# Optimization experiments

Hardware: AMD Instinct MI355X
Metric: run time of the kernel (lower is better)

## Reference

```python
import jax, jax.numpy as jnp
import numpy as np

VOCAB = 28996
B, W, D, H = 16, 64, 256, 512


def setup_inputs() -> dict:
    key = jax.random.key(0)
    ks = jax.random.split(key, 8)
    s_ih = 1.0 / np.sqrt(H)
    return {
        "x": jax.random.normal(ks[0], (B, W, D), dtype=jnp.float32),
        "last_encoder_hidden_state": jax.random.normal(ks[1], (1, H), dtype=jnp.float32),
        "w_ih": jax.random.uniform(ks[2], (3 * H, D), jnp.float32, -s_ih, s_ih),
        "w_hh": jax.random.uniform(ks[3], (3 * H, H), jnp.float32, -s_ih, s_ih),
        "b_ih": jax.random.uniform(ks[4], (3 * H,), jnp.float32, -s_ih, s_ih),
        "b_hh": jax.random.uniform(ks[5], (3 * H,), jnp.float32, -s_ih, s_ih),
        "w_pred": jax.random.uniform(ks[6], (VOCAB, H), jnp.float32, -s_ih, s_ih),
        "b_pred": jax.random.uniform(ks[7], (VOCAB,), jnp.float32, -s_ih, s_ih),
    }


def reference(x, last_encoder_hidden_state, w_ih, w_hh, b_ih, b_hh, w_pred, b_pred):
    b, w, d = x.shape
    # The torch code carries a single [1,H] hidden state sequentially over ALL
    # batch rows and words (state flows across batch boundaries). Flatten to T steps.
    xf = x.reshape(b * w, d)
    xg = xf @ w_ih.T + b_ih  # [T, 3H] input gate pre-activations, batched GEMM

    def step(h, xg_t):
        gh = h @ w_hh.T + b_hh            # [3H]
        xr, xz, xn = jnp.split(xg_t, 3)
        hr, hz, hn = jnp.split(gh, 3)
        r = jax.nn.sigmoid(xr + hr)
        z = jax.nn.sigmoid(xz + hz)
        n = jnp.tanh(xn + r * hn)
        h_new = (1.0 - z) * n + z * h
        return h_new, h_new

    h0 = last_encoder_hidden_state[0]     # [H]
    _, hs = jax.lax.scan(step, h0, xg)    # hs: [T, H]
    preds = hs @ w_pred.T + b_pred        # [T, VOCAB]
    return preds.reshape(b, w, VOCAB)
```

## Files before the change

### kernel.cpp

```cpp
#include <hip/hip_runtime.h>
#include <hip/hip_bf16.h>
#include <cstdint>

#define VOCAB 28996
#define T_STEPS 1024
#define D_IN 256
#define HDIM 512

using f32x4 = __attribute__((ext_vector_type(4))) float;
using s16x8 = __attribute__((ext_vector_type(8))) short;

static __device__ __forceinline__ unsigned short f2bf(float f){
    unsigned u = __float_as_uint(f);
    u = u + 0x7FFFu + ((u >> 16) & 1u);
    return (unsigned short)(u >> 16);
}

#define SENT_U 0x7FC00001u

__global__ void init_hs_kernel(const float* __restrict__ h0, float* __restrict__ hs,
                               unsigned* __restrict__ ctrl){
    const int col = threadIdx.x;
    const int row = blockIdx.x;
    float v = (row == 0) ? h0[col] : __uint_as_float(SENT_U);
    hs[(size_t)row * HDIM + col] = v;
    if (row == 0 && col < 8) ctrl[col] = 0u;
}

__global__ void xg_kernel(const float* __restrict__ x, const float* __restrict__ w_ih,
                          const float* __restrict__ b_ih, float* __restrict__ xg){
    __shared__ float xs[8][D_IN];
    const int tid = threadIdx.x;
    const int i   = blockIdx.x * 256 + tid;
    const int t0  = blockIdx.y * 8;
    #pragma unroll
    for (int r = 0; r < 8; ++r)
        xs[r][tid] = x[(size_t)(t0 + r) * D_IN + tid];
    __syncthreads();

    float acc[8] = {0.f,0.f,0.f,0.f,0.f,0.f,0.f,0.f};
    const float* wrow = w_ih + (size_t)i * D_IN;
    for (int d = 0; d < D_IN; d += 4){
        float4 w4 = *(const float4*)(wrow + d);
        #pragma unroll
        for (int r = 0; r < 8; ++r){
            acc[r] += w4.x * xs[r][d]   + w4.y * xs[r][d+1]
                    + w4.z * xs[r][d+2] + w4.w * xs[r][d+3];
        }
    }
    const float b = b_ih[i];
    #pragma unroll
    for (int r = 0; r < 8; ++r)
        xg[(size_t)(t0 + r) * (3*HDIM) + i] = acc[r] + b;
}

#define LDW(G, P, s) \
    float G##s##0 = (P)[128*s + 0], G##s##1 = (P)[128*s + 1], \
          G##s##2 = (P)[128*s + 2], G##s##3 = (P)[128*s + 3];
#define PINW(G, s) \
    asm volatile("" : "+v"(G##s##0), "+v"(G##s##1), "+v"(G##s##2), "+v"(G##s##3));

#define GSTEP(s, arx, azx, anx) { \
    float4 h4 = *(const float4*)&hcur[4*c + 128*s]; \
    arx += R##s##0*h4.x + R##s##1*h4.y + R##s##2*h4.z + R##s##3*h4.w; \
    azx += Z##s##0*h4.x + Z##s##1*h4.y + Z##s##2*h4.z + Z##s##3*h4.w; \
    anx += N##s##0*h4.x + N##s##1*h4.y + N##s##2*h4.z + N##s##3*h4.w; }

__launch_bounds__(512, 1)
__global__ void scan_kernel(const float* __restrict__ xg, const float* __restrict__ w_hh,
                            const float* __restrict__ b_hh, float* hs, unsigned* ctrl){
    __shared__ __align__(16) float hbuf[2][HDIM];
    __shared__ unsigned sh_rank;
    __shared__ int sh_step;

    const int tid = threadIdx.x;
    if (tid == 0){
        unsigned xcc;
        asm volatile("s_getreg_b32 %0, hwreg(HW_REG_XCC_ID)" : "=s"(xcc));
        sh_rank = __hip_atomic_fetch_add(&ctrl[xcc & 7u], 1u, __ATOMIC_RELAXED,
                                         __HIP_MEMORY_SCOPE_AGENT);
        sh_step = -1;
    }
    __syncthreads();
    const unsigned rank = sh_rank;
    if (rank >= 32u) return;

    const int wv   = tid >> 6;
    const int lane = tid & 63;
    const int c    = tid & 31;
    const int jl   = tid >> 5;
    const int j    = (int)rank * 16 + jl;

    const float* wrp = w_hh + (size_t)j * HDIM + 4*c;
    const float* wzp = w_hh + (size_t)(HDIM   + j) * HDIM + 4*c;
    const float* wnp = w_hh + (size_t)(2*HDIM + j) * HDIM + 4*c;
    LDW(R, wrp, 0) LDW(R, wrp, 1) LDW(R, wrp, 2) LDW(R, wrp, 3)
    LDW(Z, wzp, 0) LDW(Z, wzp, 1) LDW(Z, wzp, 2) LDW(Z, wzp, 3)
    LDW(N, wnp, 0) LDW(N, wnp, 1) LDW(N, wnp, 2) LDW(N, wnp, 3)
    PINW(R,0) PINW(R,1) PINW(R,2) PINW(R,3)
    PINW(Z,0) PINW(Z,1) PINW(Z,2) PINW(Z,3)
    PINW(N,0) PINW(N,1) PINW(N,2) PINW(N,3)

    float bhr = b_hh[j], bhz = b_hh[HDIM + j], bhn = b_hh[2*HDIM + j];
    asm volatile("" : "+v"(bhr), "+v"(bhz), "+v"(bhn));

    float xr_c = 0.f, xz_c = 0.f, xn_c = 0.f;
    if (c == 0){ xr_c = xg[j]; xz_c = xg[HDIM + j]; xn_c = xg[2*HDIM + j]; }

    #pragma unroll 1
    for (int t = 0; t < T_STEPS; ++t){
        float* hcur = hbuf[t & 1];

        if (wv == 0){
            const float4* myp = (const float4*)(hs + (size_t)t * HDIM) + lane;
            float4 va, vb;
            int spins = 0, dead = 0;
            for (;;){
                asm volatile("global_load_dwordx4 %0, %2, off nt\n\t"
                             "global_load_dwordx4 %1, %2, off offset:1024 nt\n\t"
                             "s_waitcnt vmcnt(0)"
                             : "=&v"(va), "=&v"(vb) : "v"(myp) : "memory");
                int ok = (__float_as_uint(va.x) != SENT_U) & (__float_as_uint(va.y) != SENT_U)
                       & (__float_as_uint(va.z) != SENT_U) & (__float_as_uint(va.w) != SENT_U)
                       & (__float_as_uint(vb.x) != SENT_U) & (__float_as_uint(vb.y) != SENT_U)
                       & (__float_as_uint(vb.z) != SENT_U) & (__float_as_uint(vb.w) != SENT_U);
                if (__all(ok)) break;
                if (++spins > 2000){ dead = 1; break; }
            }
            if (dead){
                if (lane == 0)
                    __hip_atomic_store(&sh_step, 0x7FFFFFFF, __ATOMIC_RELAXED,
                                       __HIP_MEMORY_SCOPE_WORKGROUP);
                return;
            }
            *(float4*)&hcur[4 * lane]       = va;
            *(float4*)&hcur[256 + 4 * lane] = vb;
            asm volatile("s_waitcnt lgkmcnt(0)" ::: "memory");
            if (lane == 0)
                __hip_atomic_store(&sh_step, t, __ATOMIC_RELAXED,
                                   __HIP_MEMORY_SCOPE_WORKGROUP);
        } else {
            int v;
            do {
                v = __hip_atomic_load(&sh_step, __ATOMIC_RELAXED,
                                      __HIP_MEMORY_SCOPE_WORKGROUP);
            } while (v < t);
            if (v == 0x7FFFFFFF) return;
        }
        asm volatile("" ::: "memory");
        __builtin_amdgcn_sched_barrier(0);

        float xr_n = 0.f, xz_n = 0.f, xn_n = 0.f;
        if (c == 0 && t + 1 < T_STEPS){
            const float* xgn = xg + (size_t)(t + 1) * (3*HDIM);
            xr_n = xgn[j]; xz_n = xgn[HDIM + j]; xn_n = xgn[2*HDIM + j];
        }

        float ar0=0.f, ar1=0.f, az0=0.f, az1=0.f, an0=0.f, an1=0.f;
        GSTEP(0, ar0, az0, an0)  GSTEP(1, ar1, az1, an1)
        GSTEP(2, ar0, az0, an0)  GSTEP(3, ar1, az1, an1)
        float ar = ar0 + ar1, az = az0 + az1, an = an0 + an1;
        #pragma unroll
        for (int m = 1; m < 32; m <<= 1){
            ar += __shfl_xor(ar, m);
            az += __shfl_xor(az, m);
            an += __shfl_xor(an, m);
        }

        if (c == 0){
            const float r  = 1.0f / (1.0f + __expf(-(xr_c + ar + bhr)));
            const float z  = 1.0f / (1.0f + __expf(-(xz_c + az + bhz)));
            const float nn = xn_c + r * (an + bhn);
            const float e  = __expf(2.0f * nn);
            const float th = 1.0f - 2.0f / (e + 1.0f);
            const float hnew = (1.0f - z) * th + z * hcur[j];
            hs[(size_t)(t + 1) * HDIM + j] = hnew;
        }
        xr_c = xr_n; xz_c = xz_n; xn_c = xn_n;
    }
}

__launch_bounds__(256)
__global__ void pred_gemm_kernel(const float* __restrict__ hs, const float* __restrict__ w_pred,
                                 const float* __restrict__ b_pred, float* __restrict__ out){
    __shared__ unsigned short As[128 * 32];
    __shared__ unsigned short Bs[128 * 32];
    const int tid   = threadIdx.x;
    const int mtile = blockIdx.x;
    const int ntile = blockIdx.y;
    const int row  = tid >> 1, half = tid & 1;
    const int wave = tid >> 6, lane = tid & 63;
    const int wm = wave >> 1, wn = wave & 1;
    const int lr = lane & 15, kq = lane >> 4;

    f32x4 acc[4][4] = {};

    const float* Abase = hs + HDIM  + (size_t)(mtile * 128 + row) * HDIM;
    const int    nrow  = ntile * 128 + row;
    const float* Bbase = w_pred + (size_t)nrow * HDIM;

    for (int k0 = 0; k0 < HDIM; k0 += 32){
        {
            const float* srcp = Abase + k0 + half * 16;
            unsigned short* dst = &As[row * 32 + half * 16];
            #pragma unroll
            for (int q = 0; q < 4; ++q){
                float4 v = *(const float4*)(srcp + 4 * q);
                uint2 p;
                p.x = (unsigned)f2bf(v.x) | ((unsigned)f2bf(v.y) << 16);
                p.y = (unsigned)f2bf(v.z) | ((unsigned)f2bf(v.w) << 16);
                *(uint2*)(dst + 4 * q) = p;
            }
        }
        {
            unsigned short* dst = &Bs[row * 32 + half * 16];
            if (nrow < VOCAB){
                const float* srcp = Bbase + k0 + half * 16;
                #pragma unroll
                for (int q = 0; q < 4; ++q){
                    float4 v = *(const float4*)(srcp + 4 * q);
                    uint2 p;
                    p.x = (unsigned)f2bf(v.x) | ((unsigned)f2bf(v.y) << 16);
                    p.y = (unsigned)f2bf(v.z) | ((unsigned)f2bf(v.w) << 16);
                    *(uint2*)(dst + 4 * q) = p;
                }
            } else {
                uint2 zz; zz.x = 0u; zz.y = 0u;
                #pragma unroll
                for (int q = 0; q < 4; ++q) *(uint2*)(dst + 4 * q) = zz;
            }
        }
        __syncthreads();

        const unsigned short* Ab = &As[(wm * 64 + lr) * 32 + kq * 8];
        const unsigned short* Bb = &Bs[(wn * 64 + lr) * 32 + kq * 8];
        s16x8 af[4], bf[4];
        #pragma unroll
        for (int mf = 0; mf < 4; ++mf) af[mf] = *(const s16x8*)(Ab + mf * 16 * 32);
        #pragma unroll
        for (int nf = 0; nf < 4; ++nf) bf[nf] = *(const s16x8*)(Bb + nf * 16 * 32);
        #pragma unroll
        for (int mf = 0; mf < 4; ++mf){
            #pragma unroll
            for (int nf = 0; nf < 4; ++nf){
                acc[mf][nf] = __builtin_amdgcn_mfma_f32_16x16x32_bf16(af[mf], bf[nf], acc[mf][nf], 0, 0, 0);
            }
        }
        __syncthreads();
    }

    #pragma unroll
    for (int nf = 0; nf < 4; ++nf){
        const int n = ntile * 128 + wn * 64 + nf * 16 + lr;
        if (n >= VOCAB) continue;
        const float bp = b_pred[n];
        #pragma unroll
        for (int mf = 0; mf < 4; ++mf){
            const int m = mtile * 128 + wm * 64 + mf * 16 + kq * 4;
            #pragma unroll
            for (int q = 0; q < 4; ++q){
                out[(size_t)(m + q) * VOCAB + n] = acc[mf][nf][q] + bp;
            }
        }
    }
}

extern "C" void kernel_launch(void* const* d_in, const int* in_sizes, int n_in,
                              void* d_out, int out_size, void* d_ws, size_t ws_size,
                              hipStream_t stream){
    const float* x      = (const float*)d_in[0];
    const float* h0     = (const float*)d_in[1];
    const float* w_ih   = (const float*)d_in[2];
    const float* w_hh   = (const float*)d_in[3];
    const float* b_ih   = (const float*)d_in[4];
    const float* b_hh   = (const float*)d_in[5];
    const float* w_pred = (const float*)d_in[6];
    const float* b_pred = (const float*)d_in[7];
    float* out = (float*)d_out;

    float*    xg   = (float*)d_ws;
    float*    hs   = xg + (size_t)T_STEPS * (3*HDIM);
    unsigned* ctrl = (unsigned*)(hs + (size_t)(T_STEPS+1) * HDIM);

    hipLaunchKernelGGL(init_hs_kernel, dim3(T_STEPS + 1), dim3(HDIM), 0, stream, h0, hs, ctrl);
    hipLaunchKernelGGL(xg_kernel,      dim3(6, 128),      dim3(256),  0, stream, x, w_ih, b_ih, xg);
    hipLaunchKernelGGL(scan_kernel,    dim3(256),         dim3(512),  0, stream, xg, w_hh, b_hh, hs, ctrl);
    hipLaunchKernelGGL(pred_gemm_kernel, dim3(8, 227),    dim3(256),  0, stream, hs, w_pred, b_pred, out);
}
```

Before: 1.835 ms.

## Replace NaN-sentinel polling with per-block atomic step counters for cross-block sync

The scan's cross-workgroup handoff changes from spinning on NaN sentinel values written into the hidden-state buffer to per-block counters in a control area. Each wave bumps its block's slot after its stores drain, and wave 0 polls the 32 slots with atomic adds of zero until each reaches 8*t. After that it does plain loads of the hidden row. This drops the sentinel fill of the hs buffer and the nt polling loads, and moves the next-step xg prefetch after the signal. The counter atomics use workgroup scope across blocks, which relies on same-XCC L2 coherence and could be unsafe on other placements. The launch bounds also change to waves_per_eu(2,2).

```diff
diff --git a/kernel.cpp b/kernel.cpp
--- a/kernel.cpp
+++ b/kernel.cpp
@@ -16,15 +16,15 @@
     return (unsigned short)(u >> 16);
 }
 
-#define SENT_U 0x7FC00001u
+#define CTRL_DWORDS 8224
 
 __global__ void init_hs_kernel(const float* __restrict__ h0, float* __restrict__ hs,
                                unsigned* __restrict__ ctrl){
     const int col = threadIdx.x;
     const int row = blockIdx.x;
-    float v = (row == 0) ? h0[col] : __uint_as_float(SENT_U);
-    hs[(size_t)row * HDIM + col] = v;
-    if (row == 0 && col < 8) ctrl[col] = 0u;
+    if (row == 0) hs[col] = h0[col];
+    const int idx = row * 512 + col;
+    if (idx < CTRL_DWORDS) ctrl[idx] = 0u;
 }
 
 __global__ void xg_kernel(const float* __restrict__ x, const float* __restrict__ w_ih,
@@ -66,24 +66,30 @@
     azx += Z##s##0*h4.x + Z##s##1*h4.y + Z##s##2*h4.z + Z##s##3*h4.w; \
     anx += N##s##0*h4.x + N##s##1*h4.y + N##s##2*h4.z + N##s##3*h4.w; }
 
-__launch_bounds__(512, 1)
+__launch_bounds__(512)
+__attribute__((amdgpu_waves_per_eu(2, 2)))
 __global__ void scan_kernel(const float* __restrict__ xg, const float* __restrict__ w_hh,
                             const float* __restrict__ b_hh, float* hs, unsigned* ctrl){
     __shared__ __align__(16) float hbuf[2][HDIM];
-    __shared__ unsigned sh_rank;
+    __shared__ unsigned sh_rank, sh_xcc;
     __shared__ int sh_step;
 
     const int tid = threadIdx.x;
     if (tid == 0){
         unsigned xcc;
         asm volatile("s_getreg_b32 %0, hwreg(HW_REG_XCC_ID)" : "=s"(xcc));
-        sh_rank = __hip_atomic_fetch_add(&ctrl[xcc & 7u], 1u, __ATOMIC_RELAXED,
+        xcc &= 7u;
+        sh_xcc  = xcc;
+        sh_rank = __hip_atomic_fetch_add(&ctrl[xcc], 1u, __ATOMIC_RELAXED,
                                          __HIP_MEMORY_SCOPE_AGENT);
         sh_step = -1;
     }
     __syncthreads();
     const unsigned rank = sh_rank;
     if (rank >= 32u) return;
+
+    unsigned* slots  = ctrl + 32 + (size_t)sh_xcc * 1024;
+    unsigned* myslot = slots + rank * 32;
 
     const int wv   = tid >> 6;
     const int lane = tid & 63;
@@ -104,6 +110,9 @@
     float bhr = b_hh[j], bhz = b_hh[HDIM + j], bhn = b_hh[2*HDIM + j];
     asm volatile("" : "+v"(bhr), "+v"(bhz), "+v"(bhn));
 
+    unsigned zero32 = 0u;
+    asm volatile("" : "+v"(zero32));
+
     float xr_c = 0.f, xz_c = 0.f, xn_c = 0.f;
     if (c == 0){ xr_c = xg[j]; xz_c = xg[HDIM + j]; xn_c = xg[2*HDIM + j]; }
 
@@ -112,27 +121,29 @@
         float* hcur = hbuf[t & 1];
 
         if (wv == 0){
-            const float4* myp = (const float4*)(hs + (size_t)t * HDIM) + lane;
-            float4 va, vb;
-            int spins = 0, dead = 0;
-            for (;;){
-                asm volatile("global_load_dwordx4 %0, %2, off nt\n\t"
-                             "global_load_dwordx4 %1, %2, off offset:1024 nt\n\t"
-                             "s_waitcnt vmcnt(0)"
-                             : "=&v"(va), "=&v"(vb) : "v"(myp) : "memory");
-                int ok = (__float_as_uint(va.x) != SENT_U) & (__float_as_uint(va.y) != SENT_U)
-                       & (__float_as_uint(va.z) != SENT_U) & (__float_as_uint(va.w) != SENT_U)
-                       & (__float_as_uint(vb.x) != SENT_U) & (__float_as_uint(vb.y) != SENT_U)
-                       & (__float_as_uint(vb.z) != SENT_U) & (__float_as_uint(vb.w) != SENT_U);
-                if (__all(ok)) break;
-                if (++spins > 2000){ dead = 1; break; }
-            }
-            if (dead){
-                if (lane == 0)
-                    __hip_atomic_store(&sh_step, 0x7FFFFFFF, __ATOMIC_RELAXED,
-                                       __HIP_MEMORY_SCOPE_WORKGROUP);
-                return;
-            }
+            if (t > 0){
+                int dead = 0;
+                if (lane < 32){
+                    const unsigned tgt = 8u * (unsigned)t;
+                    unsigned* sl = slots + lane * 32;
+                    int spins = 0;
+                    for (;;){
+                        unsigned v = __hip_atomic_fetch_add(sl, zero32, __ATOMIC_RELAXED,
+                                                            __HIP_MEMORY_SCOPE_WORKGROUP);
+                        if (v >= tgt) break;
+                        if (++spins > 8000){ dead = 1; break; }
+                    }
+                }
+                if (__any(dead)){
+                    if (lane == 0)
+                        __hip_atomic_store(&sh_step, 0x7FFFFFFF, __ATOMIC_RELAXED,
+                                           __HIP_MEMORY_SCOPE_WORKGROUP);
+                    return;
+                }
+            }
+            const float4* rowp = (const float4*)(hs + (size_t)t * HDIM);
+            float4 va = rowp[lane];
+            float4 vb = rowp[64 + lane];
             *(float4*)&hcur[4 * lane]       = va;
             *(float4*)&hcur[256 + 4 * lane] = vb;
             asm volatile("s_waitcnt lgkmcnt(0)" ::: "memory");
@@ -150,12 +161,6 @@
         asm volatile("" ::: "memory");
         __builtin_amdgcn_sched_barrier(0);
 
-        float xr_n = 0.f, xz_n = 0.f, xn_n = 0.f;
-        if (c == 0 && t + 1 < T_STEPS){
-            const float* xgn = xg + (size_t)(t + 1) * (3*HDIM);
-            xr_n = xgn[j]; xz_n = xgn[HDIM + j]; xn_n = xgn[2*HDIM + j];
-        }
-
         float ar0=0.f, ar1=0.f, az0=0.f, az1=0.f, an0=0.f, an1=0.f;
         GSTEP(0, ar0, az0, an0)  GSTEP(1, ar1, az1, an1)
         GSTEP(2, ar0, az0, an0)  GSTEP(3, ar1, az1, an1)
@@ -175,6 +180,16 @@
             const float th = 1.0f - 2.0f / (e + 1.0f);
             const float hnew = (1.0f - z) * th + z * hcur[j];
             hs[(size_t)(t + 1) * HDIM + j] = hnew;
+        }
+        asm volatile("s_waitcnt vmcnt(0)" ::: "memory");
+        if (lane == 0){
+            __hip_atomic_fetch_add(myslot, 1u, __ATOMIC_RELAXED,
+                                   __HIP_MEMORY_SCOPE_WORKGROUP);
+        }
+        float xr_n = 0.f, xz_n = 0.f, xn_n = 0.f;
+        if (c == 0 && t + 1 < T_STEPS){
+            const float* xgn = xg + (size_t)(t + 1) * (3*HDIM);
+            xr_n = xgn[j]; xz_n = xgn[HDIM + j]; xn_n = xgn[2*HDIM + j];
         }
         xr_c = xr_n; xz_c = xz_n; xn_c = xn_n;
     }
```

New measurement: 2.482 ms. +35.2%, slower.

## Poll hidden state directly from global memory in every wave, dropping LDS handoff

Applied to the files above, without the earlier changes.

Each wave of the persistent GRU scan now spins on the global hidden-state row itself, loading its four float4 slices plus its own h[j] with nontemporal loads. This replaces the single loader wave that staged the row into a shared-memory double buffer and released the other waves through an LDS step flag. The goal is to remove the intra-block handoff latency from the per-step critical path. The trade-off is eight times more polling traffic to L2 per block, and the next-step xg prefetch now sits after the gate math instead of overlapping the dot products. Launch bounds also change to request two waves per EU.

```diff
diff --git a/kernel.cpp b/kernel.cpp
--- a/kernel.cpp
+++ b/kernel.cpp
@@ -60,18 +60,16 @@
 #define PINW(G, s) \
     asm volatile("" : "+v"(G##s##0), "+v"(G##s##1), "+v"(G##s##2), "+v"(G##s##3));
 
-#define GSTEP(s, arx, azx, anx) { \
-    float4 h4 = *(const float4*)&hcur[4*c + 128*s]; \
-    arx += R##s##0*h4.x + R##s##1*h4.y + R##s##2*h4.z + R##s##3*h4.w; \
-    azx += Z##s##0*h4.x + Z##s##1*h4.y + Z##s##2*h4.z + Z##s##3*h4.w; \
-    anx += N##s##0*h4.x + N##s##1*h4.y + N##s##2*h4.z + N##s##3*h4.w; }
-
-__launch_bounds__(512, 1)
+#define GS(s, hh) { \
+    ar += R##s##0*hh.x + R##s##1*hh.y + R##s##2*hh.z + R##s##3*hh.w; \
+    az += Z##s##0*hh.x + Z##s##1*hh.y + Z##s##2*hh.z + Z##s##3*hh.w; \
+    an += N##s##0*hh.x + N##s##1*hh.y + N##s##2*hh.z + N##s##3*hh.w; }
+
+__launch_bounds__(512)
+__attribute__((amdgpu_waves_per_eu(2, 2)))
 __global__ void scan_kernel(const float* __restrict__ xg, const float* __restrict__ w_hh,
                             const float* __restrict__ b_hh, float* hs, unsigned* ctrl){
-    __shared__ __align__(16) float hbuf[2][HDIM];
     __shared__ unsigned sh_rank;
-    __shared__ int sh_step;
 
     const int tid = threadIdx.x;
     if (tid == 0){
@@ -79,17 +77,14 @@
         asm volatile("s_getreg_b32 %0, hwreg(HW_REG_XCC_ID)" : "=s"(xcc));
         sh_rank = __hip_atomic_fetch_add(&ctrl[xcc & 7u], 1u, __ATOMIC_RELAXED,
                                          __HIP_MEMORY_SCOPE_AGENT);
-        sh_step = -1;
     }
     __syncthreads();
     const unsigned rank = sh_rank;
     if (rank >= 32u) return;
 
-    const int wv   = tid >> 6;
-    const int lane = tid & 63;
-    const int c    = tid & 31;
-    const int jl   = tid >> 5;
-    const int j    = (int)rank * 16 + jl;
+    const int c  = tid & 31;
+    const int jl = tid >> 5;
+    const int j  = (int)rank * 16 + jl;
 
     const float* wrp = w_hh + (size_t)j * HDIM + 4*c;
     const float* wzp = w_hh + (size_t)(HDIM   + j) * HDIM + 4*c;
@@ -107,59 +102,39 @@
     float xr_c = 0.f, xz_c = 0.f, xn_c = 0.f;
     if (c == 0){ xr_c = xg[j]; xz_c = xg[HDIM + j]; xn_c = xg[2*HDIM + j]; }
 
+    const float* lanep = hs + 4*c;
+    const float* jp    = hs + j;
+
     #pragma unroll 1
     for (int t = 0; t < T_STEPS; ++t){
-        float* hcur = hbuf[t & 1];
-
-        if (wv == 0){
-            const float4* myp = (const float4*)(hs + (size_t)t * HDIM) + lane;
-            float4 va, vb;
-            int spins = 0, dead = 0;
-            for (;;){
-                asm volatile("global_load_dwordx4 %0, %2, off nt\n\t"
-                             "global_load_dwordx4 %1, %2, off offset:1024 nt\n\t"
-                             "s_waitcnt vmcnt(0)"
-                             : "=&v"(va), "=&v"(vb) : "v"(myp) : "memory");
-                int ok = (__float_as_uint(va.x) != SENT_U) & (__float_as_uint(va.y) != SENT_U)
-                       & (__float_as_uint(va.z) != SENT_U) & (__float_as_uint(va.w) != SENT_U)
-                       & (__float_as_uint(vb.x) != SENT_U) & (__float_as_uint(vb.y) != SENT_U)
-                       & (__float_as_uint(vb.z) != SENT_U) & (__float_as_uint(vb.w) != SENT_U);
-                if (__all(ok)) break;
-                if (++spins > 2000){ dead = 1; break; }
-            }
-            if (dead){
-                if (lane == 0)
-                    __hip_atomic_store(&sh_step, 0x7FFFFFFF, __ATOMIC_RELAXED,
-                                       __HIP_MEMORY_SCOPE_WORKGROUP);
-                return;
-            }
-            *(float4*)&hcur[4 * lane]       = va;
-            *(float4*)&hcur[256 + 4 * lane] = vb;
-            asm volatile("s_waitcnt lgkmcnt(0)" ::: "memory");
-            if (lane == 0)
-                __hip_atomic_store(&sh_step, t, __ATOMIC_RELAXED,
-                                   __HIP_MEMORY_SCOPE_WORKGROUP);
-        } else {
-            int v;
-            do {
-                v = __hip_atomic_load(&sh_step, __ATOMIC_RELAXED,
-                                      __HIP_MEMORY_SCOPE_WORKGROUP);
-            } while (v < t);
-            if (v == 0x7FFFFFFF) return;
-        }
-        asm volatile("" ::: "memory");
-        __builtin_amdgcn_sched_barrier(0);
-
-        float xr_n = 0.f, xz_n = 0.f, xn_n = 0.f;
-        if (c == 0 && t + 1 < T_STEPS){
-            const float* xgn = xg + (size_t)(t + 1) * (3*HDIM);
-            xr_n = xgn[j]; xz_n = xgn[HDIM + j]; xn_n = xgn[2*HDIM + j];
-        }
-
-        float ar0=0.f, ar1=0.f, az0=0.f, az1=0.f, an0=0.f, an1=0.f;
-        GSTEP(0, ar0, az0, an0)  GSTEP(1, ar1, az1, an1)
-        GSTEP(2, ar0, az0, an0)  GSTEP(3, ar1, az1, an1)
-        float ar = ar0 + ar1, az = az0 + az1, an = an0 + an1;
+        f32x4 h0, h1, h2, h3;
+        float hj;
+        int spins = 0;
+        for (;;){
+            asm volatile(
+                "global_load_dwordx4 %0, %5, off nt\n\t"
+                "global_load_dwordx4 %1, %5, off offset:512 nt\n\t"
+                "global_load_dwordx4 %2, %5, off offset:1024 nt\n\t"
+                "global_load_dwordx4 %3, %5, off offset:1536 nt\n\t"
+                "global_load_dword   %4, %6, off nt\n\t"
+                "s_waitcnt vmcnt(0)"
+                : "=&v"(h0), "=&v"(h1), "=&v"(h2), "=&v"(h3), "=&v"(hj)
+                : "v"(lanep), "v"(jp) : "memory");
+            int ok = (__float_as_uint(h0.x) != SENT_U) & (__float_as_uint(h0.y) != SENT_U)
+                   & (__float_as_uint(h0.z) != SENT_U) & (__float_as_uint(h0.w) != SENT_U)
+                   & (__float_as_uint(h1.x) != SENT_U) & (__float_as_uint(h1.y) != SENT_U)
+                   & (__float_as_uint(h1.z) != SENT_U) & (__float_as_uint(h1.w) != SENT_U)
+                   & (__float_as_uint(h2.x) != SENT_U) & (__float_as_uint(h2.y) != SENT_U)
+                   & (__float_as_uint(h2.z) != SENT_U) & (__float_as_uint(h2.w) != SENT_U)
+                   & (__float_as_uint(h3.x) != SENT_U) & (__float_as_uint(h3.y) != SENT_U)
+                   & (__float_as_uint(h3.z) != SENT_U) & (__float_as_uint(h3.w) != SENT_U)
+                   & (__float_as_uint(hj)   != SENT_U);
+            if (__all(ok)) break;
+            if (++spins > 4000) return;
+        }
+
+        float ar = 0.f, az = 0.f, an = 0.f;
+        GS(0, h0) GS(1, h1) GS(2, h2) GS(3, h3)
         #pragma unroll
         for (int m = 1; m < 32; m <<= 1){
             ar += __shfl_xor(ar, m);
@@ -173,10 +148,19 @@
             const float nn = xn_c + r * (an + bhn);
             const float e  = __expf(2.0f * nn);
             const float th = 1.0f - 2.0f / (e + 1.0f);
-            const float hnew = (1.0f - z) * th + z * hcur[j];
+            const float hnew = (1.0f - z) * th + z * hj;
             hs[(size_t)(t + 1) * HDIM + j] = hnew;
         }
+
+        float xr_n = 0.f, xz_n = 0.f, xn_n = 0.f;
+        if (c == 0 && t + 1 < T_STEPS){
+            const float* xgn = xg + (size_t)(t + 1) * (3*HDIM);
+            xr_n = xgn[j]; xz_n = xgn[HDIM + j]; xn_n = xgn[2*HDIM + j];
+        }
         xr_c = xr_n; xz_c = xz_n; xn_c = xn_n;
+
+        lanep += HDIM;
+        jp    += HDIM;
     }
 }
 
```

Measured after the change: 1.789 ms. -2.5%, faster.
